# Kernel tuning notes

Hardware: AMD Instinct MI355X
Metric: run time of the kernel (lower is better)

Reference implementation:

```python
import jax, jax.numpy as jnp
import numpy as np

NR, NC = 30, 20  # grid rows/cols
H = W = 512
B = 4
CIN = 55

def _conv(x, w, b, dil, pad):
    y = jax.lax.conv_general_dilated(
        x, w, window_strides=(1, 1), padding=[(pad, pad), (pad, pad)],
        rhs_dilation=(dil, dil), dimension_numbers=('NCHW', 'OIHW', 'NCHW'))
    return y + b[None, :, None, None]

def _cell_means(t, cell, n_cells):
    # t: [B,C,H,W]; torch.mean over the WHOLE slice (batch+channel+cell pixels)
    b, c = t.shape[0], t.shape[1]
    s = t.sum(axis=(0, 1))                              # [H,W]
    sums = jax.ops.segment_sum(s.ravel(), cell.ravel(), num_segments=n_cells)
    cnts = jax.ops.segment_sum(jnp.ones((t.shape[2] * t.shape[3],), t.dtype),
                               cell.ravel(), num_segments=n_cells) * (b * c)
    return sums / cnts                                   # [n_cells]

def setup_inputs() -> dict:
    key = jax.random.key(0)
    ks = jax.random.split(key, 16)
    x = jax.random.normal(ks[0], (B, CIN, H, W), jnp.float32)
    # segment ids per row/col, nondecreasing, every id present
    row_seg = jnp.sort(jnp.concatenate([jnp.arange(NR, dtype=jnp.int32),
                                        jax.random.randint(ks[1], (H - NR,), 0, NR, jnp.int32)]))
    col_seg = jnp.sort(jnp.concatenate([jnp.arange(NC, dtype=jnp.int32),
                                        jax.random.randint(ks[2], (W - NC,), 0, NC, jnp.int32)]))
    def wb(k, o, i, kh, kw):
        fan = i * kh * kw
        lim = 1.0 / np.sqrt(fan)
        k1, k2 = jax.random.split(k)
        w = jax.random.uniform(k1, (o, i, kh, kw), jnp.float32, -lim, lim)
        b = jax.random.uniform(k2, (o,), jnp.float32, -lim, lim)
        return w, b
    w1, b1 = wb(ks[3], 6, CIN, 5, 5)
    w2, b2 = wb(ks[4], 6, CIN, 5, 5)
    w3, b3 = wb(ks[5], 6, CIN, 5, 5)
    wt, bt = wb(ks[6], 36, 18, 1, 1)
    wbm, bbm = wb(ks[7], 1, 18, 1, 1)
    return {'x': x, 'row_seg': row_seg, 'col_seg': col_seg,
            'w1': w1, 'b1': b1, 'w2': w2, 'b2': b2, 'w3': w3, 'b3': b3,
            'wt': wt, 'bt': bt, 'wb': wbm, 'bb': bbm}

def reference(x, row_seg, col_seg, w1, b1, w2, b2, w3, b3, wt, bt, wb, bb):
    x1 = jax.nn.relu(_conv(x, w1, b1, 1, 2))
    x2 = jax.nn.relu(_conv(x, w2, b2, 2, 4))
    x3 = jax.nn.relu(_conv(x, w3, b3, 3, 6))
    feat = jnp.concatenate([x1, x2, x3], axis=1)          # [B,18,H,W]
    top = _conv(feat, wt, bt, 1, 0)                        # [B,36,H,W]
    bot = _conv(feat, wb, bb, 1, 0)                        # [B,1,H,W]
    cell = row_seg[:, None] * NC + col_seg[None, :]        # [H,W]
    n_cells = NR * NC
    top_m = _cell_means(top, cell, n_cells)                # [600]
    bot_m = _cell_means(bot, cell, n_cells)                # [600]
    b = x.shape[0]
    top_out = jnp.broadcast_to(top_m[cell][None, None], (b, top.shape[1], top.shape[2], top.shape[3]))
    bot_out = jnp.broadcast_to(bot_m[cell][None, None], (b, 1, bot.shape[2], bot.shape[3]))
    pools = jnp.broadcast_to(jax.nn.sigmoid(bot_m).reshape(1, 1, NR, NC), (b, 1, NR, NC))
    out_x = jnp.concatenate([top_out, feat, jax.nn.sigmoid(bot_out)], axis=1)  # [B,55,H,W]
    return out_x, pools
```

## Files before the change

### kernel.cpp

```cpp
#include <hip/hip_runtime.h>
#include <math.h>

#define HW 512
#define NPIX (HW*HW)
#define NB 4
#define NCIN 55
#define OUTX_SIZE (NB*55*NPIX)

#define WA_OFF 0
#define WSUM_OFF 37632
#define BTSUM_OFF 37650
#define S_OFF 37664
#define TM_OFF 38864
#define SBM_OFF 39464

#define BY 16
#define BX 32
#define LROWS 28
#define LCOLS 48
#define LSTRIDE 49
#define CELLS (LROWS*LSTRIDE)
#define LDSC 1536
#define NSTEP 7
#define NCB 7

#define PH 524
#define PW 528
#define CBBYTES (PH*PW*16)

typedef _Float16 half2v __attribute__((ext_vector_type(2)));
typedef __attribute__((ext_vector_type(8))) _Float16 f16x8;
typedef __attribute__((ext_vector_type(4))) float f32x4;

__device__ __forceinline__ uint pack_f16x2(float a, float b) {
  return __builtin_bit_cast(uint, __builtin_amdgcn_cvt_pkrtz(a, b));
}

__device__ __forceinline__ void gload16(const void* g, void* l) {
  __builtin_amdgcn_global_load_lds(
      (const __attribute__((address_space(1))) void*)g,
      (__attribute__((address_space(3))) void*)l, 16, 0, 0);
}

__global__ __launch_bounds__(1024) void prep_kernel(
    const float* __restrict__ w1, const float* __restrict__ w2, const float* __restrict__ w3,
    const float* __restrict__ wt, const float* __restrict__ bt,
    float* __restrict__ ws)
{
  const int t = threadIdx.x;
  uint* wp = (uint*)(ws + WA_OFF);
  for (int e = t; e < 3 * NCB * NSTEP * 64 * 4; e += 1024) {
    int u = e & 3;
    int rest = e >> 2;
    int lane = rest & 63;
    int idx = rest >> 6;
    int step = idx % 7;
    int cbg = idx / 7;
    int cb = cbg % 7;
    int g = cbg / 7;
    int oc = lane & 15;
    int kg = lane >> 4;
    int tap = step * 4 + kg;
    int c = cb * 8 + 2 * u;
    const float* wsrc = (g == 0) ? w1 : (g == 1) ? w2 : w3;
    float lo = 0.f, hi = 0.f;
    if (oc < 6 && tap < 25) {
      if (c < NCIN)     lo = wsrc[(oc * NCIN + c) * 25 + tap];
      if (c + 1 < NCIN) hi = wsrc[(oc * NCIN + c + 1) * 25 + tap];
    }
    wp[e] = pack_f16x2(lo, hi);
  }
  if (t < 18) {
    float s = 0.f;
    for (int o = 0; o < 36; o++) s += wt[o * 18 + t];
    ws[WSUM_OFF + t] = s;
  }
  if (t == 18) {
    float s = 0.f;
    for (int o = 0; o < 36; o++) s += bt[o];
    ws[BTSUM_OFF] = s;
  }
  for (int e = t; e < 1200; e += 1024) ws[S_OFF + e] = 0.f;
}

__global__ __launch_bounds__(256) void prepack_kernel(
    const float* __restrict__ x, float* __restrict__ out)
{
  const uint idx = blockIdx.x * 256 + threadIdx.x;
  const uint pw = idx % PW;
  const uint r1 = idx / PW;
  const uint py = r1 % PH;
  const uint r2 = r1 / PH;
  const uint cb = r2 % 7;
  const uint b  = r2 / 7;
  const int gy = (int)py - 6, gx = (int)pw - 8;
  const bool in = ((unsigned)gy < (unsigned)HW) && ((unsigned)gx < (unsigned)HW);
  const int c0 = cb * 8;
  float v[8];
#pragma unroll
  for (int q = 0; q < 8; q++) {
    v[q] = (in && (c0 + q < NCIN))
         ? x[(((size_t)(b * NCIN + c0 + q)) << 18) + (size_t)gy * HW + gx]
         : 0.f;
  }
  uint4 u;
  u.x = pack_f16x2(v[0], v[1]); u.y = pack_f16x2(v[2], v[3]);
  u.z = pack_f16x2(v[4], v[5]); u.w = pack_f16x2(v[6], v[7]);
  char* dst = (char*)(out + ((size_t)(b * 55) << 18))
            + (size_t)cb * CBBYTES + ((size_t)py * PW + pw) * 16;
  *(uint4*)dst = u;
}

__global__ __launch_bounds__(256, 2) void conv_kernel(
    const uint* wA, const float* bias1, const float* bias2,
    const float* bias3, float* out)
{
  __shared__ uint xs[2 * LDSC * 4];
  const int tid = threadIdx.x;
  const int lane = tid & 63;
  const int wv = tid >> 6;
  const int h0 = blockIdx.y * BY, w0 = blockIdx.x * BX;
  const int bz = blockIdx.z;
  const int col = lane & 15;
  const int kg  = lane >> 4;

  const char* xb = (const char*)out + (((size_t)(bz * 55)) << 20);
  const uint4* wA4 = (const uint4*)wA;

  uint voff[6];
#pragma unroll
  for (int t = 0; t < 6; t++) {
    int l = (wv * 6 + t) * 64 + lane;
    if (l > CELLS - 1) l = CELLS - 1;
    int row = l / LSTRIDE;
    int c = l - row * LSTRIDE;
    if (c > LCOLS - 1) c = LCOLS - 1;
    voff[t] = (uint)(((h0 + row) * PW) + (w0 + c)) * 16u;
  }

  int so[3][7];
#pragma unroll
  for (int g = 0; g < 3; g++) {
#pragma unroll
    for (int s = 0; s < 7; s++) {
      int tap = s * 4 + kg;
      int dr = 0, dc = 0;
      if (tap < 25) { int q5 = tap / 5; dr = q5 - 2; dc = tap - q5 * 5 - 2; }
      so[g][s] = ((dr * LSTRIDE + dc) * (g + 1)) << 2;
    }
  }

  f32x4 acc[3][8];
#pragma unroll
  for (int g = 0; g < 3; g++)
#pragma unroll
    for (int nt = 0; nt < 8; nt++) acc[g][nt] = (f32x4){0.f, 0.f, 0.f, 0.f};

  {
    const char* sb = xb;
    uint* db = xs;
#pragma unroll
    for (int t = 0; t < 6; t++)
      gload16(sb + voff[t], (char*)db + ((wv * 6 + t) * 1024));
  }
  __syncthreads();

  int cur = 0;
#pragma unroll 1
  for (int cb = 0; cb < NCB; cb++) {
    if (cb < NCB - 1) {
      const char* sb = xb + (size_t)(cb + 1) * CBBYTES;
      uint* db = xs + (cur ^ 1) * (LDSC * 4);
#pragma unroll
      for (int t = 0; t < 6; t++)
        gload16(sb + voff[t], (char*)db + ((wv * 6 + t) * 1024));
    }
    const uint* xsb = xs + cur * (LDSC * 4);
#pragma unroll
    for (int g = 0; g < 3; g++) {
      const uint4* wp4 = wA4 + (size_t)((g * NCB + cb) * NSTEP) * 64 + lane;
      f16x8 af[7];
#pragma unroll
      for (int s = 0; s < 7; s++)
        af[s] = __builtin_bit_cast(f16x8, wp4[(size_t)s * 64]);
#pragma unroll
      for (int nt = 0; nt < 8; nt++) {
        const int bd = (((6 + (wv << 2) + (nt >> 1)) * LSTRIDE)
                       + (8 + ((nt & 1) << 4) + col)) << 2;
        f32x4 a = acc[g][nt];
#pragma unroll
        for (int s = 0; s < 7; s++) {
          uint4 tv = *(const uint4*)&xsb[bd + so[g][s]];
          a = __builtin_amdgcn_mfma_f32_16x16x32_f16(
                af[s], __builtin_bit_cast(f16x8, tv), a, 0, 0, 0);
        }
        acc[g][nt] = a;
      }
    }
    __syncthreads();
    cur ^= 1;
  }

#pragma unroll
  for (int g = 0; g < 3; g++) {
    const float* bp = (g == 0) ? bias1 : (g == 1) ? bias2 : bias3;
    float bsel[4];
#pragma unroll
    for (int r = 0; r < 4; r++) {
      int slot = (kg << 2) + r;
      bsel[r] = (slot < 6) ? bp[slot] : 0.f;
    }
#pragma unroll
    for (int nt = 0; nt < 8; nt++) {
      const int y = h0 + (wv << 2) + (nt >> 1);
      const int xx = w0 + ((nt & 1) << 4) + col;
      const size_t pix = (size_t)y * HW + xx;
#pragma unroll
      for (int r = 0; r < 4; r++) {
        int slot = (kg << 2) + r;
        if (slot < 6) {
          int ch = 36 + g * 6 + slot;
          out[(((size_t)(bz * 55 + ch)) << 18) + pix] =
              fmaxf(acc[g][nt][r] + bsel[r], 0.f);
        }
      }
    }
  }
}

__global__ __launch_bounds__(256) void cellsum_kernel(
    const float* __restrict__ out, const int* __restrict__ row_seg,
    const int* __restrict__ col_seg, const float* __restrict__ wsum,
    const float* __restrict__ wb, float* __restrict__ S)
{
  __shared__ float part[40];
  const int tid = threadIdx.x;
  const int h = blockIdx.y;
  const int w = blockIdx.x * 256 + tid;
  if (tid < 40) part[tid] = 0.f;
  __syncthreads();
  float st = 0.f, sb = 0.f;
  const size_t pix = (size_t)h * HW + w;
#pragma unroll
  for (int b = 0; b < NB; b++)
#pragma unroll
    for (int k = 0; k < 18; k++) {
      float v = out[(((size_t)(b * 55 + 36 + k)) << 18) + pix];
      st = fmaf(wsum[k], v, st);
      sb = fmaf(wb[k], v, sb);
    }
  int cs = col_seg[w];
  atomicAdd(&part[cs * 2], st);
  atomicAdd(&part[cs * 2 + 1], sb);
  __syncthreads();
  if (tid < 20) {
    int cell = row_seg[h] * 20 + tid;
    atomicAdd(&S[cell * 2], part[tid * 2]);
    atomicAdd(&S[cell * 2 + 1], part[tid * 2 + 1]);
  }
}

__global__ __launch_bounds__(1024) void finalize_kernel(
    const int* __restrict__ row_seg, const int* __restrict__ col_seg,
    const float* __restrict__ S, const float* __restrict__ btsum,
    const float* __restrict__ bb, float* __restrict__ tm,
    float* __restrict__ sbm, float* __restrict__ out)
{
  __shared__ int rowcnt[30], colcnt[20];
  const int t = threadIdx.x;
  if (t < 30) rowcnt[t] = 0;
  if (t >= 32 && t < 52) colcnt[t - 32] = 0;
  __syncthreads();
  if (t < 512) atomicAdd(&rowcnt[row_seg[t]], 1);
  else atomicAdd(&colcnt[col_seg[t - 512]], 1);
  __syncthreads();
  if (t < 600) {
    int r = t / 20, c = t - r * 20;
    float cnt = (float)(rowcnt[r] * colcnt[c]);
    float topm = S[2 * t] / (cnt * 144.f) + btsum[0] * (1.f / 36.f);
    float botm = S[2 * t + 1] / (cnt * 4.f) + bb[0];
    tm[t] = topm;
    float s = 1.f / (1.f + expf(-botm));
    sbm[t] = s;
#pragma unroll
    for (int b = 0; b < 4; b++) out[OUTX_SIZE + b * 600 + t] = s;
  }
}

__global__ __launch_bounds__(256) void fill_kernel(
    const int* __restrict__ row_seg, const int* __restrict__ col_seg,
    const float* __restrict__ tm, const float* __restrict__ sbm,
    float* __restrict__ out)
{
  const int idx = blockIdx.x * 256 + threadIdx.x;
  const int b = idx >> 16;
  const int p4 = idx & 65535;
  const int h = p4 >> 7, w = (p4 & 127) << 2;
  const int rs = row_seg[h] * 20;
  float4 tmv, sbv;
  {
    int c0 = rs + col_seg[w + 0];
    int c1 = rs + col_seg[w + 1];
    int c2 = rs + col_seg[w + 2];
    int c3 = rs + col_seg[w + 3];
    tmv.x = tm[c0]; tmv.y = tm[c1]; tmv.z = tm[c2]; tmv.w = tm[c3];
    sbv.x = sbm[c0]; sbv.y = sbm[c1]; sbv.z = sbm[c2]; sbv.w = sbm[c3];
  }
  const size_t hw = (size_t)h * HW + w;
  float* base = out + (((size_t)(b * 55)) << 18) + hw;
#pragma unroll
  for (int ch = 0; ch < 36; ch++) *(float4*)(base + ((size_t)ch << 18)) = tmv;
  *(float4*)(base + ((size_t)54 << 18)) = sbv;
}

extern "C" void kernel_launch(void* const* d_in, const int* in_sizes, int n_in,
                              void* d_out, int out_size, void* d_ws, size_t ws_size,
                              hipStream_t stream) {
  const float* x       = (const float*)d_in[0];
  const int*   row_seg = (const int*)d_in[1];
  const int*   col_seg = (const int*)d_in[2];
  const float* w1 = (const float*)d_in[3];
  const float* b1 = (const float*)d_in[4];
  const float* w2 = (const float*)d_in[5];
  const float* b2 = (const float*)d_in[6];
  const float* w3 = (const float*)d_in[7];
  const float* b3 = (const float*)d_in[8];
  const float* wt = (const float*)d_in[9];
  const float* bt = (const float*)d_in[10];
  const float* wb = (const float*)d_in[11];
  const float* bb = (const float*)d_in[12];
  float* out = (float*)d_out;
  float* ws  = (float*)d_ws;

  prep_kernel<<<1, 1024, 0, stream>>>(w1, w2, w3, wt, bt, ws);

  prepack_kernel<<<(NB * 7 * PH * PW) / 256, 256, 0, stream>>>(x, out);

  dim3 g1(HW / BX, HW / BY, NB);
  conv_kernel<<<g1, 256, 0, stream>>>((const uint*)(ws + WA_OFF),
                                      b1, b2, b3, out);

  dim3 g2(HW / 256, HW);
  cellsum_kernel<<<g2, 256, 0, stream>>>(out, row_seg, col_seg,
                                         ws + WSUM_OFF, wb, ws + S_OFF);

  finalize_kernel<<<1, 1024, 0, stream>>>(row_seg, col_seg, ws + S_OFF,
                                          ws + BTSUM_OFF, bb,
                                          ws + TM_OFF, ws + SBM_OFF, out);

  fill_kernel<<<NB * NPIX / 1024, 256, 0, stream>>>(row_seg, col_seg,
                                                    ws + TM_OFF, ws + SBM_OFF, out);
}
```

Measured before the change: 678.4 us.

## Fuse cell-sum reduction into conv epilogue and merge prep with vectorized prepack

Folds the per-cell weighted sums into the conv kernel's epilogue, using LDS bins and global atomics, so the 18 feature channels are not reread by a separate cellsum kernel. The weight prep is merged into the prepack launch, and prepack now loads float4s and writes four pixels per thread. The LDS tile drops to the 22 loads actually needed, and occupancy hint rises to 3 blocks per CU. The cost is 4.8KB of extra LDS per block, a zeroing pass, and more global atomics on the 1200 cell sums.

Measured after the change: 700.4 us. +3.2%, slower.

```diff
diff --git a/kernel.cpp b/kernel.cpp
--- a/kernel.cpp
+++ b/kernel.cpp
@@ -17,16 +17,19 @@
 #define BY 16
 #define BX 32
 #define LROWS 28
-#define LCOLS 48
 #define LSTRIDE 49
 #define CELLS (LROWS*LSTRIDE)
-#define LDSC 1536
+#define NLD 22
+#define LDSC 1408
 #define NSTEP 7
 #define NCB 7
 
 #define PH 524
 #define PW 528
 #define CBBYTES (PH*PW*16)
+
+#define PREP_WBLK 147
+#define PPK_TOT (NB*7*PH*(PW/4))
 
 typedef _Float16 half2v __attribute__((ext_vector_type(2)));
 typedef __attribute__((ext_vector_type(8))) _Float16 f16x8;
@@ -42,14 +45,17 @@
       (__attribute__((address_space(3))) void*)l, 16, 0, 0);
 }
 
-__global__ __launch_bounds__(1024) void prep_kernel(
+__global__ __launch_bounds__(256) void prep_prepack_kernel(
+    const float* __restrict__ x,
     const float* __restrict__ w1, const float* __restrict__ w2, const float* __restrict__ w3,
     const float* __restrict__ wt, const float* __restrict__ bt,
-    float* __restrict__ ws)
+    float* __restrict__ ws, float* __restrict__ out)
 {
-  const int t = threadIdx.x;
-  uint* wp = (uint*)(ws + WA_OFF);
-  for (int e = t; e < 3 * NCB * NSTEP * 64 * 4; e += 1024) {
+  const int blk = blockIdx.x;
+  const int tid = threadIdx.x;
+  if (blk < PREP_WBLK) {
+    const int e = blk * 256 + tid;
+    uint* wp = (uint*)(ws + WA_OFF);
     int u = e & 3;
     int rest = e >> 2;
     int lane = rest & 63;
@@ -69,53 +75,64 @@
       if (c + 1 < NCIN) hi = wsrc[(oc * NCIN + c + 1) * 25 + tap];
     }
     wp[e] = pack_f16x2(lo, hi);
-  }
-  if (t < 18) {
-    float s = 0.f;
-    for (int o = 0; o < 36; o++) s += wt[o * 18 + t];
-    ws[WSUM_OFF + t] = s;
-  }
-  if (t == 18) {
-    float s = 0.f;
-    for (int o = 0; o < 36; o++) s += bt[o];
-    ws[BTSUM_OFF] = s;
-  }
-  for (int e = t; e < 1200; e += 1024) ws[S_OFF + e] = 0.f;
-}
-
-__global__ __launch_bounds__(256) void prepack_kernel(
-    const float* __restrict__ x, float* __restrict__ out)
-{
-  const uint idx = blockIdx.x * 256 + threadIdx.x;
-  const uint pw = idx % PW;
-  const uint r1 = idx / PW;
-  const uint py = r1 % PH;
-  const uint r2 = r1 / PH;
-  const uint cb = r2 % 7;
-  const uint b  = r2 / 7;
-  const int gy = (int)py - 6, gx = (int)pw - 8;
-  const bool in = ((unsigned)gy < (unsigned)HW) && ((unsigned)gx < (unsigned)HW);
+    if (e < 1200) ws[S_OFF + e] = 0.f;
+    if (blk == 0) {
+      if (tid < 18) {
+        float s = 0.f;
+        for (int o = 0; o < 36; o++) s += wt[o * 18 + tid];
+        ws[WSUM_OFF + tid] = s;
+      }
+      if (tid == 18) {
+        float s = 0.f;
+        for (int o = 0; o < 36; o++) s += bt[o];
+        ws[BTSUM_OFF] = s;
+      }
+    }
+    return;
+  }
+  const uint idx = (uint)(blk - PREP_WBLK) * 256u + (uint)tid;
+  if (idx >= (uint)PPK_TOT) return;
+  const uint pw4 = idx % 132u;
+  const uint r1 = idx / 132u;
+  const uint py = r1 % 524u;
+  const uint r2 = r1 / 524u;
+  const uint cb = r2 % 7u;
+  const uint b  = r2 / 7u;
+  const int gy = (int)py - 6;
+  const int gx = (int)(pw4 << 2) - 8;
+  const bool in = ((unsigned)gy < (unsigned)HW) && (gx >= 0) && (gx < HW);
   const int c0 = cb * 8;
-  float v[8];
+  float4 f[8];
 #pragma unroll
   for (int q = 0; q < 8; q++) {
-    v[q] = (in && (c0 + q < NCIN))
-         ? x[(((size_t)(b * NCIN + c0 + q)) << 18) + (size_t)gy * HW + gx]
-         : 0.f;
-  }
-  uint4 u;
-  u.x = pack_f16x2(v[0], v[1]); u.y = pack_f16x2(v[2], v[3]);
-  u.z = pack_f16x2(v[4], v[5]); u.w = pack_f16x2(v[6], v[7]);
+    float4 fz; fz.x = fz.y = fz.z = fz.w = 0.f;
+    f[q] = (in && (c0 + q < NCIN))
+         ? *(const float4*)(x + (((size_t)(b * NCIN + c0 + q)) << 18)
+                              + (size_t)gy * HW + gx)
+         : fz;
+  }
+  const float* fp = (const float*)&f[0];
   char* dst = (char*)(out + ((size_t)(b * 55) << 18))
-            + (size_t)cb * CBBYTES + ((size_t)py * PW + pw) * 16;
-  *(uint4*)dst = u;
-}
-
-__global__ __launch_bounds__(256, 2) void conv_kernel(
-    const uint* wA, const float* bias1, const float* bias2,
-    const float* bias3, float* out)
+            + (size_t)cb * CBBYTES + ((size_t)py * PW + (pw4 << 2)) * 16;
+#pragma unroll
+  for (int p = 0; p < 4; p++) {
+    uint4 u;
+    u.x = pack_f16x2(fp[0 * 4 + p], fp[1 * 4 + p]);
+    u.y = pack_f16x2(fp[2 * 4 + p], fp[3 * 4 + p]);
+    u.z = pack_f16x2(fp[4 * 4 + p], fp[5 * 4 + p]);
+    u.w = pack_f16x2(fp[6 * 4 + p], fp[7 * 4 + p]);
+    *(uint4*)(dst + p * 16) = u;
+  }
+}
+
+__global__ __launch_bounds__(256, 3) void conv_kernel(
+    const uint* wA, const float* bias1, const float* bias2, const float* bias3,
+    const int* __restrict__ row_seg, const int* __restrict__ col_seg,
+    const float* __restrict__ wsum18, const float* __restrict__ wb18,
+    float* __restrict__ S, float* out)
 {
   __shared__ uint xs[2 * LDSC * 4];
+  __shared__ float bins[1200];
   const int tid = threadIdx.x;
   const int lane = tid & 63;
   const int wv = tid >> 6;
@@ -127,14 +144,17 @@
   const char* xb = (const char*)out + (((size_t)(bz * 55)) << 20);
   const uint4* wA4 = (const uint4*)wA;
 
+  for (int e = tid; e < 1200; e += 256) bins[e] = 0.f;
+
   uint voff[6];
 #pragma unroll
   for (int t = 0; t < 6; t++) {
-    int l = (wv * 6 + t) * 64 + lane;
+    int ld = wv * 6 + t;
+    int l = ld * 64 + lane;
     if (l > CELLS - 1) l = CELLS - 1;
     int row = l / LSTRIDE;
     int c = l - row * LSTRIDE;
-    if (c > LCOLS - 1) c = LCOLS - 1;
+    if (c > 47) c = 47;
     voff[t] = (uint)(((h0 + row) * PW) + (w0 + c)) * 16u;
   }
 
@@ -156,12 +176,10 @@
 #pragma unroll
     for (int nt = 0; nt < 8; nt++) acc[g][nt] = (f32x4){0.f, 0.f, 0.f, 0.f};
 
-  {
-    const char* sb = xb;
-    uint* db = xs;
-#pragma unroll
-    for (int t = 0; t < 6; t++)
-      gload16(sb + voff[t], (char*)db + ((wv * 6 + t) * 1024));
+#pragma unroll
+  for (int t = 0; t < 6; t++) {
+    int ld = wv * 6 + t;
+    if (ld < NLD) gload16(xb + voff[t], (char*)xs + ld * 1024);
   }
   __syncthreads();
 
@@ -170,10 +188,12 @@
   for (int cb = 0; cb < NCB; cb++) {
     if (cb < NCB - 1) {
       const char* sb = xb + (size_t)(cb + 1) * CBBYTES;
-      uint* db = xs + (cur ^ 1) * (LDSC * 4);
-#pragma unroll
-      for (int t = 0; t < 6; t++)
-        gload16(sb + voff[t], (char*)db + ((wv * 6 + t) * 1024));
+      char* db = (char*)(xs + (cur ^ 1) * (LDSC * 4));
+#pragma unroll
+      for (int t = 0; t < 6; t++) {
+        int ld = wv * 6 + t;
+        if (ld < NLD) gload16(sb + voff[t], db + ld * 1024);
+      }
     }
     const uint* xsb = xs + cur * (LDSC * 4);
 #pragma unroll
@@ -201,62 +221,52 @@
     cur ^= 1;
   }
 
+  float bsel[3][4], wsl[3][4], wbl[3][4];
 #pragma unroll
   for (int g = 0; g < 3; g++) {
     const float* bp = (g == 0) ? bias1 : (g == 1) ? bias2 : bias3;
-    float bsel[4];
 #pragma unroll
     for (int r = 0; r < 4; r++) {
       int slot = (kg << 2) + r;
-      bsel[r] = (slot < 6) ? bp[slot] : 0.f;
-    }
-#pragma unroll
-    for (int nt = 0; nt < 8; nt++) {
-      const int y = h0 + (wv << 2) + (nt >> 1);
-      const int xx = w0 + ((nt & 1) << 4) + col;
-      const size_t pix = (size_t)y * HW + xx;
+      bsel[g][r] = (slot < 6) ? bp[slot] : 0.f;
+      wsl[g][r]  = (slot < 6) ? wsum18[g * 6 + slot] : 0.f;
+      wbl[g][r]  = (slot < 6) ? wb18[g * 6 + slot] : 0.f;
+    }
+  }
+#pragma unroll
+  for (int nt = 0; nt < 8; nt++) {
+    const int y = h0 + (wv << 2) + (nt >> 1);
+    const int xx = w0 + ((nt & 1) << 4) + col;
+    const size_t pix = (size_t)y * HW + xx;
+    float stv = 0.f, sbv = 0.f;
+#pragma unroll
+    for (int g = 0; g < 3; g++) {
 #pragma unroll
       for (int r = 0; r < 4; r++) {
         int slot = (kg << 2) + r;
         if (slot < 6) {
+          float v = fmaxf(acc[g][nt][r] + bsel[g][r], 0.f);
           int ch = 36 + g * 6 + slot;
-          out[(((size_t)(bz * 55 + ch)) << 18) + pix] =
-              fmaxf(acc[g][nt][r] + bsel[r], 0.f);
+          out[(((size_t)(bz * 55 + ch)) << 18) + pix] = v;
+          stv = fmaf(wsl[g][r], v, stv);
+          sbv = fmaf(wbl[g][r], v, sbv);
         }
       }
     }
-  }
-}
-
-__global__ __launch_bounds__(256) void cellsum_kernel(
-    const float* __restrict__ out, const int* __restrict__ row_seg,
-    const int* __restrict__ col_seg, const float* __restrict__ wsum,
-    const float* __restrict__ wb, float* __restrict__ S)
-{
-  __shared__ float part[40];
-  const int tid = threadIdx.x;
-  const int h = blockIdx.y;
-  const int w = blockIdx.x * 256 + tid;
-  if (tid < 40) part[tid] = 0.f;
+    stv += __shfl_xor(stv, 16);
+    stv += __shfl_xor(stv, 32);
+    sbv += __shfl_xor(sbv, 16);
+    sbv += __shfl_xor(sbv, 32);
+    if (lane < 16) {
+      int cell = row_seg[y] * 20 + col_seg[xx];
+      atomicAdd(&bins[cell * 2], stv);
+      atomicAdd(&bins[cell * 2 + 1], sbv);
+    }
+  }
   __syncthreads();
-  float st = 0.f, sb = 0.f;
-  const size_t pix = (size_t)h * HW + w;
-#pragma unroll
-  for (int b = 0; b < NB; b++)
-#pragma unroll
-    for (int k = 0; k < 18; k++) {
-      float v = out[(((size_t)(b * 55 + 36 + k)) << 18) + pix];
-      st = fmaf(wsum[k], v, st);
-      sb = fmaf(wb[k], v, sb);
-    }
-  int cs = col_seg[w];
-  atomicAdd(&part[cs * 2], st);
-  atomicAdd(&part[cs * 2 + 1], sb);
-  __syncthreads();
-  if (tid < 20) {
-    int cell = row_seg[h] * 20 + tid;
-    atomicAdd(&S[cell * 2], part[tid * 2]);
-    atomicAdd(&S[cell * 2 + 1], part[tid * 2 + 1]);
+  for (int e = tid; e < 1200; e += 256) {
+    float v = bins[e];
+    if (v != 0.f) atomicAdd(&S[e], v);
   }
 }
 
@@ -332,17 +342,14 @@
   float* out = (float*)d_out;
   float* ws  = (float*)d_ws;
 
-  prep_kernel<<<1, 1024, 0, stream>>>(w1, w2, w3, wt, bt, ws);
-
-  prepack_kernel<<<(NB * 7 * PH * PW) / 256, 256, 0, stream>>>(x, out);
+  const int ppk_blocks = PREP_WBLK + (PPK_TOT + 255) / 256;
+  prep_prepack_kernel<<<ppk_blocks, 256, 0, stream>>>(x, w1, w2, w3, wt, bt,
+                                                      ws, out);
 
   dim3 g1(HW / BX, HW / BY, NB);
   conv_kernel<<<g1, 256, 0, stream>>>((const uint*)(ws + WA_OFF),
-                                      b1, b2, b3, out);
-
-  dim3 g2(HW / 256, HW);
-  cellsum_kernel<<<g2, 256, 0, stream>>>(out, row_seg, col_seg,
-                                         ws + WSUM_OFF, wb, ws + S_OFF);
+                                      b1, b2, b3, row_seg, col_seg,
+                                      ws + WSUM_OFF, wb, ws + S_OFF, out);
 
   finalize_kernel<<<1, 1024, 0, stream>>>(row_seg, col_seg, ws + S_OFF,
                                           ws + BTSUM_OFF, bb,
```
